# Optimization experiments

Measured on AMD Instinct MI355X. Metric: run time of the kernel, lower is better.

Reference implementation:

```python
import jax, jax.numpy as jnp
import numpy as np

H = 256; S = 64; AN = 16; D = 8; HH = 8; WW = 8; T = 32; N = 64; NV = 32
HG = 2 + 3 * H  # GRU hidden = sum(parser_sections) = 1 + 1 + 3*H


def _gru(x, w_ih, w_hh, b_ih, b_hh):
    """torch-style GRU over leading axis; x: [L, N, Hin] -> [L, N, HG]."""
    def step(h, xt):
        gi = xt @ w_ih.T + b_ih
        gh = h @ w_hh.T + b_hh
        ir, iz, inn = jnp.split(gi, 3, axis=-1)
        hr, hz, hn = jnp.split(gh, 3, axis=-1)
        r = jax.nn.sigmoid(ir + hr)
        z = jax.nn.sigmoid(iz + hz)
        n = jnp.tanh(inn + r * hn)
        h2 = (1 - z) * n + z * h
        return h2, h2
    h0 = jnp.zeros((x.shape[1], w_hh.shape[1]), x.dtype)
    _, ys = jax.lax.scan(step, h0, x)
    return ys


def _cos(e, m):  # e [N,H], m [N,S,H] -> [N,S]; matches F.cosine_similarity eps=1e-8
    num = jnp.einsum('nh,nsh->ns', e, m)
    den = jnp.linalg.norm(e, axis=-1)[:, None] * jnp.linalg.norm(m, axis=-1)
    return num / jnp.maximum(den, 1e-8)


def _l1norm(x):  # F.normalize(x, p=1, dim=-1)
    return x / jnp.maximum(jnp.abs(x).sum(-1, keepdims=True), 1e-12)


def setup_inputs():
    key = jax.random.key(0)
    ks = jax.random.split(key, 16)
    sc = lambda k, shape, fan: jax.random.normal(k, shape, jnp.float32) / np.float32(np.sqrt(fan))
    return dict(
        base=jax.random.normal(ks[0], (T, N, D, HH, WW), jnp.float32),
        interactable=(jax.random.uniform(ks[1], (T, N, AN - 5)) < 0.5).astype(jnp.float32),
        rnn_hxs=jnp.zeros((1, N, 1 + AN + 1 + H + S), jnp.float32),
        emb=sc(ks[2], (NV, H), 1.0),
        gru_w_ih=sc(ks[3], (3 * HG, H), H),
        gru_w_hh=sc(ks[4], (3 * HG, HG), HG),
        gru_b_ih=jnp.zeros((3 * HG,), jnp.float32),
        gru_b_hh=jnp.zeros((3 * HG,), jnp.float32),
        conv0_w=sc(ks[5], (H, D * H), D * H),
        conv0_b=jnp.zeros((H,), jnp.float32),
        convs_w=sc(ks[6], (2, H, H), H),
        convs_b=jnp.zeros((2, H), jnp.float32),
        lin_w=sc(ks[7], (H, H * HH * WW), H * HH * WW),
        lin_b=jnp.zeros((H,), jnp.float32),
        psi_w=sc(ks[8], (H, H * AN), H * AN),
        psi_b=jnp.zeros((H,), jnp.float32),
        actor_w=sc(ks[9], (AN, H), H),
        actor_b=jnp.zeros((AN,), jnp.float32),
        critic_w=sc(ks[10], (1, H), H),
        critic_b=jnp.zeros((1,), jnp.float32),
        subtasks=jax.random.randint(ks[11], (N, S), 0, NV),
        actions=jax.random.randint(ks[12], (T, N), 0, AN),
    )


def reference(base, interactable, rnn_hxs, emb, gru_w_ih, gru_w_hh, gru_b_ih, gru_b_hh,
              conv0_w, conv0_b, convs_w, convs_b, lin_w, lin_b, psi_w, psi_b,
              actor_w, actor_b, critic_w, critic_b, subtasks, actions):
    # --- parser: GRU over the subtask token sequence ---
    rnn_in = emb[subtasks].transpose(1, 0, 2)                                    # [S, N, H]
    X = _gru(rnn_in, gru_w_ih, gru_w_hh, gru_b_ih, gru_b_hh).transpose(1, 0, 2)  # [N, S, HG]
    c, p0 = X[..., 0], X[..., 1]                                                 # [N, S]
    M = X[..., 2:2 + H]
    Mm = X[..., 2 + H:2 + 2 * H]
    Mp = X[..., 2 + 2 * H:]
    hx = rnn_hxs[0]
    new_ep = jnp.all(rnn_hxs == 0, axis=-1)[0]                                   # [N]
    p_init = jnp.where(new_ep[:, None], p0, hx[:, 1 + AN + 1 + H:])

    def f_net(base_t, r):
        n = base_t.shape[0]
        # outer product [N,H,d,h,w] -> [N, H*d, h, w], then 1x1 convs
        x = (base_t[:, None] * r[:, :, None, None, None]).reshape(n, H * D, HH, WW)
        x = jax.nn.relu(jnp.einsum('nchw,oc->nohw', x, conv0_w) + conv0_b[None, :, None, None])
        for i in range(convs_w.shape[0]):
            x = jax.nn.relu(jnp.einsum('nchw,oc->nohw', x, convs_w[i]) + convs_b[i][None, :, None, None])
        return jax.nn.relu(x.reshape(n, -1) @ lin_w.T + lin_b)

    def step(p, xs):
        base_t, inter_t, a_t = xs
        ps = jax.nn.softmax(p, axis=-1)
        r = jnp.einsum('ns,nsh->nh', ps, M)                                      # memory read
        s = f_net(base_t, r)
        dprobs = jax.nn.softmax(s @ actor_w.T + actor_b, axis=-1)
        nonzero = jnp.pad(inter_t, ((0, 0), (5, 0)), constant_values=1.0)        # [N, AN]
        probs = dprobs * nonzero
        deficit = 1.0 - probs.sum(-1, keepdims=True)
        probs = probs + _l1norm(nonzero) * deficit
        probs = _l1norm(jnp.clip(probs, 0.0, 1.0))
        a_oh = jax.nn.one_hot(a_t, AN, dtype=s.dtype)
        e = (s[:, :, None] * a_oh[:, None, :]).reshape(s.shape[0], H * AN) @ psi_w.T + psi_b
        p_new = ps + c * _cos(e, Mp) - c * _cos(e, Mm)                           # memory write
        v = s @ critic_w.T + critic_b
        out = jnp.concatenate([a_t[:, None].astype(s.dtype), probs, v, s, p_new], axis=-1)
        return p_new, out

    _, hx_out = jax.lax.scan(step, p_init, (base, interactable, actions))        # [T, N, 338]
    return hx_out, hx_out[-1:]
```

## Files before the change

### kernel.cpp

```cpp
#include <hip/hip_runtime.h>
#include <math.h>

constexpr int cH  = 256;
constexpr int cS  = 64;
constexpr int cAN = 16;
constexpr int cD  = 8;
constexpr int cT  = 32;
constexpr int cN  = 64;
constexpr int cHG = 770;
constexpr int cG3 = 2310;
constexpr int cOW = 338;
constexpr int XLD = 800;
constexpr int GLD = 832;
constexpr int MLD = 2496;

__global__ __launch_bounds__(256) void k_gitab(const float* __restrict__ emb,
                                               const float* __restrict__ w_ih,
                                               const float* __restrict__ b_ih,
                                               float* __restrict__ gitp) {
  int v = blockIdx.y;
  int j = blockIdx.x * 256 + threadIdx.x;
  __shared__ float es[cH];
  es[threadIdx.x] = emb[v * cH + threadIdx.x];
  __syncthreads();
  if (j < cG3) {
    float acc = b_ih[j];
    const float* wr = w_ih + (size_t)j * cH;
    #pragma unroll 8
    for (int h = 0; h < cH; ++h) acc += wr[h] * es[h];
    int g = j / cHG, kk = j - g * cHG;
    gitp[(size_t)v * MLD + g * GLD + kk] = acc;
  }
}

__global__ __launch_bounds__(256) void k_wpad(const float* __restrict__ whh,
                                              float* __restrict__ wpadG) {
  int idx = blockIdx.x * 256 + threadIdx.x;
  if (idx < MLD * XLD) {
    int row = idx / XLD, col = idx - row * XLD;
    int g = row / GLD, k = row - g * GLD;
    wpadG[idx] = (k < cHG && col < cHG) ? whh[(size_t)(g * cHG + k) * cHG + col] : 0.f;
  }
}

__global__ __launch_bounds__(256) void k_psiperm(const float* __restrict__ psi_w,
                                                 float* __restrict__ psip) {
  int idx = blockIdx.x * 256 + threadIdx.x;
  int a = idx >> 16, h = (idx >> 8) & 255, o = idx & 255;
  psip[idx] = psi_w[((size_t)o * cH + h) * cAN + a];
}

__global__ __launch_bounds__(256) void k_gru_gemm(const float* __restrict__ wpadG,
                                                  const float* __restrict__ X,
                                                  float* __restrict__ part, int s) {
  int tid = threadIdx.x;
  int tile = blockIdx.x % 39;
  int ks   = blockIdx.x / 39;
  int g = tile / 13, kt = tile - g * 13;
  int cbase = (ks <= 2) ? ks * 13 : 38;
  int ccnt  = (ks < 2) ? 13 : 12;
  int kbase = cbase * 16;
  int csz = ccnt * 16;

  __shared__ float Bst[208][68];
  __shared__ float As[2][16][68];

  const float* bsrc = wpadG + ((size_t)(g * GLD + kt * 64)) * XLD + kbase;
  for (int i = tid; i < 64 * 208; i += 256) {
    int jl = i / 208, k2l = i - jl * 208;
    if (k2l < csz) Bst[k2l][jl] = bsrc[(size_t)jl * XLD + k2l];
  }

  int tm = tid & 15, tj = tid >> 4;
  int lrow = tid >> 2, lcol = (tid & 3) * 4;
  __syncthreads();

  float acc[4][4] = {};
  const float* Xp = X + ((size_t)lrow * cS + (s - 1)) * XLD + kbase;
  float4 av = *(const float4*)(Xp + lcol);
  for (int c = 0; c < ccnt; ++c) {
    int buf = c & 1;
    As[buf][lcol + 0][lrow] = av.x;
    As[buf][lcol + 1][lrow] = av.y;
    As[buf][lcol + 2][lrow] = av.z;
    As[buf][lcol + 3][lrow] = av.w;
    __syncthreads();
    if (c + 1 < ccnt) av = *(const float4*)(Xp + (c + 1) * 16 + lcol);
    #pragma unroll
    for (int kk = 0; kk < 16; ++kk) {
      float4 a4 = *(const float4*)&As[buf][kk][tm * 4];
      float4 b4 = *(const float4*)&Bst[c * 16 + kk][tj * 4];
      acc[0][0] += a4.x * b4.x; acc[0][1] += a4.x * b4.y; acc[0][2] += a4.x * b4.z; acc[0][3] += a4.x * b4.w;
      acc[1][0] += a4.y * b4.x; acc[1][1] += a4.y * b4.y; acc[1][2] += a4.y * b4.z; acc[1][3] += a4.y * b4.w;
      acc[2][0] += a4.z * b4.x; acc[2][1] += a4.z * b4.y; acc[2][2] += a4.z * b4.z; acc[2][3] += a4.z * b4.w;
      acc[3][0] += a4.w * b4.x; acc[3][1] += a4.w * b4.y; acc[3][2] += a4.w * b4.z; acc[3][3] += a4.w * b4.w;
    }
    __syncthreads();
  }
  float* pw = part + (size_t)ks * (64 * MLD) + (size_t)(g * GLD + kt * 64);
  #pragma unroll
  for (int i = 0; i < 4; ++i) {
    *(float4*)(pw + (size_t)(tm * 4 + i) * MLD + tj * 4) =
        make_float4(acc[i][0], acc[i][1], acc[i][2], acc[i][3]);
  }
}

__global__ __launch_bounds__(256) void k_gru_gate(const float* __restrict__ part,
                                                  const float* __restrict__ bhh,
                                                  const float* __restrict__ gitp,
                                                  const int* __restrict__ subtasks,
                                                  float* __restrict__ X, int s) {
  int kq = blockIdx.x, m = blockIdx.y, tid = threadIdx.x;
  if (tid >= 200) return;
  int k = kq * 200 + tid;
  float* xrow = X + ((size_t)m * cS + s) * XLD;
  if (k >= cHG) { xrow[k] = 0.f; return; }
  float accr = 0.f, accz = 0.f, accn = 0.f;
  if (s > 0) {
    const float* pm = part + (size_t)m * MLD;
    #pragma unroll
    for (int q = 0; q < 4; ++q) {
      const float* pq = pm + (size_t)q * (64 * MLD);
      accr += pq[k];
      accz += pq[GLD + k];
      accn += pq[2 * GLD + k];
    }
  }
  int v = subtasks[m * cS + s];
  const float* git = gitp + (size_t)v * MLD;
  float rg = 1.f / (1.f + expf(-(git[k]           + accr + bhh[k])));
  float zg = 1.f / (1.f + expf(-(git[GLD + k]     + accz + bhh[cHG + k])));
  float ng = tanhf(git[2 * GLD + k] + rg * (accn + bhh[2 * cHG + k]));
  float hp = (s > 0) ? X[((size_t)m * cS + (s - 1)) * XLD + k] : 0.f;
  xrow[k] = (1.f - zg) * ng + zg * hp;
}

__global__ __launch_bounds__(256) void k_pinit(const float* __restrict__ hxs,
                                               const float* __restrict__ X,
                                               float* __restrict__ psb,
                                               float* __restrict__ r,
                                               float* __restrict__ nMp,
                                               float* __restrict__ nMm) {
  int n = blockIdx.x, tid = threadIdx.x;
  __shared__ int anynz;
  __shared__ float pss[cS];
  __shared__ float mx, sm;
  if (tid == 0) anynz = 0;
  __syncthreads();
  int nz = (hxs[n * cOW + tid] != 0.f) ? 1 : 0;
  if (tid + 256 < cOW) nz |= (hxs[n * cOW + tid + 256] != 0.f) ? 1 : 0;
  if (nz) anynz = 1;
  __syncthreads();
  bool newep = (anynz == 0);
  if (tid < cS) {
    const float* xr = X + ((size_t)n * cS + tid) * XLD;
    float p0 = xr[1];
    float pv = newep ? p0 : hxs[n * cOW + 1 + cAN + 1 + cH + tid];
    pss[tid] = pv;
    float sp = 0.f, smn = 0.f;
    for (int h = 0; h < cH; ++h) {
      float vp = xr[2 + 2 * cH + h]; sp += vp * vp;
      float vm = xr[2 + cH + h];     smn += vm * vm;
    }
    nMp[n * cS + tid] = sqrtf(sp);
    nMm[n * cS + tid] = sqrtf(smn);
  }
  __syncthreads();
  if (tid == 0) { float m = pss[0]; for (int i = 1; i < cS; ++i) m = fmaxf(m, pss[i]); mx = m; }
  __syncthreads();
  if (tid < cS) pss[tid] = expf(pss[tid] - mx);
  __syncthreads();
  if (tid == 0) { float s = 0.f; for (int i = 0; i < cS; ++i) s += pss[i]; sm = s; }
  __syncthreads();
  if (tid < cS) { pss[tid] /= sm; psb[n * cS + tid] = pss[tid]; }
  __syncthreads();
  float acc = 0.f;
  for (int s2 = 0; s2 < cS; ++s2)
    acc += pss[s2] * X[((size_t)n * cS + s2) * XLD + 2 + tid];
  r[n * cH + tid] = acc;
}

__global__ __launch_bounds__(256) void k_front(const float* __restrict__ r,
                                               const float* __restrict__ base,
                                               const float* __restrict__ cw,
                                               const float* __restrict__ cb,
                                               float* __restrict__ x1T, int t) {
  int o = blockIdx.x, tid = threadIdx.x;
  __shared__ float rsQ[64][65][4];
  __shared__ float w0s[64][9];

  #pragma unroll
  for (int it = 0; it < 16; ++it) {
    int flat4 = it * 256 + tid;
    int n = flat4 >> 6, hq = flat4 & 63;
    float4 v = *(const float4*)(r + n * cH + hq * 4);
    *(float4*)&rsQ[hq][n][0] = v;
  }
  __syncthreads();

  {
    int dg = tid >> 6, n = tid & 63;
    int d0 = dg * 2;
    const float* cwo = cw + (size_t)o * (cD * cH);
    float acc0 = 0.f, acc1 = 0.f;
    #pragma unroll 4
    for (int hq = 0; hq < 64; ++hq) {
      float4 rv = *(const float4*)&rsQ[hq][n][0];
      #pragma unroll
      for (int j = 0; j < 4; ++j) {
        float2 w = *(const float2*)(cwo + (hq * 4 + j) * 8 + d0);
        float rvj = ((const float*)&rv)[j];
        acc0 += w.x * rvj;
        acc1 += w.y * rvj;
      }
    }
    w0s[n][d0]     = acc0;
    w0s[n][d0 + 1] = acc1;
  }
  __syncthreads();

  {
    int q = tid >> 6, n = tid & 63;
    float w0[8];
    #pragma unroll
    for (int d = 0; d < 8; ++d) w0[d] = w0s[n][d];
    float bias = cb[o];
    const float4* b4 = (const float4*)(base + ((size_t)(t * cN + n) * cD) * 64);
    float* dst = x1T + (size_t)o * 4096 + n * 64 + q * 16;
    #pragma unroll
    for (int k = 0; k < 4; ++k) {
      float4 acc = make_float4(bias, bias, bias, bias);
      #pragma unroll
      for (int d = 0; d < 8; ++d) {
        float4 bv = b4[d * 16 + q * 4 + k];
        acc.x += w0[d] * bv.x; acc.y += w0[d] * bv.y;
        acc.z += w0[d] * bv.z; acc.w += w0[d] * bv.w;
      }
      acc.x = fmaxf(acc.x, 0.f); acc.y = fmaxf(acc.y, 0.f);
      acc.z = fmaxf(acc.z, 0.f); acc.w = fmaxf(acc.w, 0.f);
      *(float4*)(dst + k * 4) = acc;
    }
  }
}

__global__ __launch_bounds__(256) void k_gemmT(const float* __restrict__ AT,
                                               const float* __restrict__ W,
                                               const float* __restrict__ bias,
                                               float* __restrict__ C, int mode) {
  int nb = blockIdx.x, mb = blockIdx.y, tid = threadIdx.x;
  int tm = tid & 15, tj = tid >> 4;
  __shared__ float As[16][68];
  __shared__ float Bs[16][68];
  float acc[4][4] = {{0.f}};
  int lrow = tid >> 2, lcol = (tid & 3) * 4;
  int kr = tid >> 4, mc4 = (tid & 15) * 4;
  for (int kc = 0; kc < cH; kc += 16) {
    float4 av = *(const float4*)(AT + (size_t)(kc + kr) * 4096 + mb * 64 + mc4);
    float4 wv = *(const float4*)(W + (size_t)(nb * 64 + lrow) * cH + kc + lcol);
    *(float4*)&As[kr][mc4] = av;
    Bs[lcol][lrow] = wv.x; Bs[lcol + 1][lrow] = wv.y; Bs[lcol + 2][lrow] = wv.z; Bs[lcol + 3][lrow] = wv.w;
    __syncthreads();
    #pragma unroll
    for (int kk = 0; kk < 16; ++kk) {
      float4 a4 = *(const float4*)&As[kk][tm * 4];
      float4 b4 = *(const float4*)&Bs[kk][tj * 4];
      acc[0][0] += a4.x * b4.x; acc[0][1] += a4.x * b4.y; acc[0][2] += a4.x * b4.z; acc[0][3] += a4.x * b4.w;
      acc[1][0] += a4.y * b4.x; acc[1][1] += a4.y * b4.y; acc[1][2] += a4.y * b4.z; acc[1][3] += a4.y * b4.w;
      acc[2][0] += a4.z * b4.x; acc[2][1] += a4.z * b4.y; acc[2][2] += a4.z * b4.z; acc[2][3] += a4.z * b4.w;
      acc[3][0] += a4.w * b4.x; acc[3][1] += a4.w * b4.y; acc[3][2] += a4.w * b4.z; acc[3][3] += a4.w * b4.w;
    }
    __syncthreads();
  }
  if (mode == 0) {
    #pragma unroll
    for (int j = 0; j < 4; ++j) {
      int o = nb * 64 + tj * 4 + j;
      float bv = bias[o];
      float4 o4;
      o4.x = fmaxf(acc[0][j] + bv, 0.f);
      o4.y = fmaxf(acc[1][j] + bv, 0.f);
      o4.z = fmaxf(acc[2][j] + bv, 0.f);
      o4.w = fmaxf(acc[3][j] + bv, 0.f);
      *(float4*)(C + (size_t)o * 4096 + mb * 64 + tm * 4) = o4;
    }
  } else {
    #pragma unroll
    for (int j = 0; j < 4; ++j) {
      int o = nb * 64 + tj * 4 + j;
      float bv = bias[o];
      float4 o4;
      o4.x = fmaxf(acc[0][j] + bv, 0.f);
      o4.y = fmaxf(acc[1][j] + bv, 0.f);
      o4.z = fmaxf(acc[2][j] + bv, 0.f);
      o4.w = fmaxf(acc[3][j] + bv, 0.f);
      *(float4*)(C + (size_t)mb * (64 * cH) + (size_t)o * 64 + tm * 4) = o4;
    }
  }
}

__global__ __launch_bounds__(256) void k_lin(const float* __restrict__ A,
                                             const float* __restrict__ W,
                                             float* __restrict__ part) {
  int nb = blockIdx.x, kcb = blockIdx.y, tid = threadIdx.x;
  int tm = tid & 15, tj = tid >> 4;
  __shared__ float As[16][68];
  __shared__ float Bs[16][68];
  float acc[4][4] = {{0.f}};
  int lrow = tid >> 2, lcol = (tid & 3) * 4;
  for (int kc = 0; kc < 256; kc += 16) {
    float4 av = *(const float4*)(A + (size_t)lrow * 16384 + kcb * 256 + kc + lcol);
    float4 wv = *(const float4*)(W + (size_t)(nb * 64 + lrow) * 16384 + kcb * 256 + kc + lcol);
    As[lcol][lrow] = av.x; As[lcol + 1][lrow] = av.y; As[lcol + 2][lrow] = av.z; As[lcol + 3][lrow] = av.w;
    Bs[lcol][lrow] = wv.x; Bs[lcol + 1][lrow] = wv.y; Bs[lcol + 2][lrow] = wv.z; Bs[lcol + 3][lrow] = wv.w;
    __syncthreads();
    #pragma unroll
    for (int kk = 0; kk < 16; ++kk) {
      float4 a4 = *(const float4*)&As[kk][tm * 4];
      float4 b4 = *(const float4*)&Bs[kk][tj * 4];
      acc[0][0] += a4.x * b4.x; acc[0][1] += a4.x * b4.y; acc[0][2] += a4.x * b4.z; acc[0][3] += a4.x * b4.w;
      acc[1][0] += a4.y * b4.x; acc[1][1] += a4.y * b4.y; acc[1][2] += a4.y * b4.z; acc[1][3] += a4.y * b4.w;
      acc[2][0] += a4.z * b4.x; acc[2][1] += a4.z * b4.y; acc[2][2] += a4.z * b4.z; acc[2][3] += a4.z * b4.w;
      acc[3][0] += a4.w * b4.x; acc[3][1] += a4.w * b4.y; acc[3][2] += a4.w * b4.z; acc[3][3] += a4.w * b4.w;
    }
    __syncthreads();
  }
  #pragma unroll
  for (int i = 0; i < 4; ++i) {
    int n = tm * 4 + i;
    float4 o4 = make_float4(acc[i][0], acc[i][1], acc[i][2], acc[i][3]);
    *(float4*)(part + ((size_t)kcb * cN + n) * cH + nb * 64 + tj * 4) = o4;
  }
}

__global__ __launch_bounds__(256) void k_tail(const float* __restrict__ part,
                                              const float* __restrict__ lin_b,
                                              const float* __restrict__ actor_w,
                                              const float* __restrict__ actor_b,
                                              const float* __restrict__ critic_w,
                                              const float* __restrict__ critic_b,
                                              const float* __restrict__ psip,
                                              const float* __restrict__ psi_b,
                                              const float* __restrict__ inter,
                                              const int* __restrict__ actions,
                                              const float* __restrict__ X,
                                              const float* __restrict__ nMp,
                                              const float* __restrict__ nMm,
                                              float* __restrict__ psb,
                                              float* __restrict__ r,
                                              float* __restrict__ out, int t) {
  int n = blockIdx.x, tid = threadIdx.x;
  __shared__ float ss[cH];
  __shared__ float es[cH];
  __shared__ float lg[cAN], dp[cAN], nzv[cAN], prb[cAN];
  __shared__ float red[256];
  __shared__ float ared[16][17];
  __shared__ float enorm_s;
  __shared__ float pns[cS];
  __shared__ float mx2, sm2;
  float* orow = out + ((size_t)t * cN + n) * cOW;
  float acc = lin_b[tid];
  for (int kc = 0; kc < 64; ++kc) acc += part[((size_t)kc * cN + n) * cH + tid];
  float sv = fmaxf(acc, 0.f);
  ss[tid] = sv;
  orow[1 + cAN + 1 + tid] = sv;
  __syncthreads();
  {
    int a = tid & 15, hg = tid >> 4;
    float pa = 0.f;
    const float* wr = actor_w + a * cH + hg * 16;
    const float* sh = &ss[hg * 16];
    #pragma unroll
    for (int hh2 = 0; hh2 < 16; ++hh2) pa += wr[hh2] * sh[hh2];
    ared[a][hg] = pa;
  }
  __syncthreads();
  if (tid < cAN) {
    float a = actor_b[tid];
    #pragma unroll
    for (int i = 0; i < 16; ++i) a += ared[tid][i];
    lg[tid] = a;
  }
  __syncthreads();
  if (tid < cAN) {
    float m = lg[0];
    for (int i = 1; i < cAN; ++i) m = fmaxf(m, lg[i]);
    dp[tid] = expf(lg[tid] - m);
  }
  __syncthreads();
  if (tid < cAN) {
    float s = 0.f;
    for (int i = 0; i < cAN; ++i) s += dp[i];
    float dprob = dp[tid] / s;
    float nv = (tid < 5) ? 1.f : inter[((size_t)t * cN + n) * (cAN - 5) + (tid - 5)];
    nzv[tid] = nv;
    prb[tid] = dprob * nv;
  }
  __syncthreads();
  if (tid < cAN) {
    float sp = 0.f, sn = 0.f;
    for (int i = 0; i < cAN; ++i) { sp += prb[i]; sn += nzv[i]; }
    float deficit = 1.f - sp;
    float v2 = prb[tid] + (nzv[tid] / fmaxf(sn, 1e-12f)) * deficit;
    prb[tid] = fminf(fmaxf(v2, 0.f), 1.f);
  }
  __syncthreads();
  if (tid < cAN) {
    float s = 0.f;
    for (int i = 0; i < cAN; ++i) s += prb[i];
    orow[1 + tid] = prb[tid] / fmaxf(s, 1e-12f);
  }
  int at = actions[t * cN + n];
  {
    float a = psi_b[tid];
    for (int h = 0; h < cH; ++h) a += psip[((size_t)at * cH + h) * cH + tid] * ss[h];
    es[tid] = a;
    red[tid] = a * a;
  }
  __syncthreads();
  for (int st = 128; st > 0; st >>= 1) {
    if (tid < st) red[tid] += red[tid + st];
    __syncthreads();
  }
  if (tid == 0) enorm_s = sqrtf(red[0]);
  __syncthreads();
  float enorm = enorm_s;
  red[tid] = critic_w[tid] * ss[tid];
  __syncthreads();
  for (int st = 128; st > 0; st >>= 1) {
    if (tid < st) red[tid] += red[tid + st];
    __syncthreads();
  }
  if (tid == 0) {
    orow[1 + cAN] = red[0] + critic_b[0];
    orow[0] = (float)at;
  }
  if (tid < cS) {
    const float* xr = X + ((size_t)n * cS + tid) * XLD;
    float dpp = 0.f, dmm = 0.f;
    for (int h = 0; h < cH; ++h) {
      float ev = es[h];
      dpp += ev * xr[2 + 2 * cH + h];
      dmm += ev * xr[2 + cH + h];
    }
    float cP = dpp / fmaxf(enorm * nMp[n * cS + tid], 1e-8f);
    float cM = dmm / fmaxf(enorm * nMm[n * cS + tid], 1e-8f);
    float cc = xr[0];
    float pn = psb[n * cS + tid] + cc * cP - cc * cM;
    pns[tid] = pn;
    orow[1 + cAN + 1 + cH + tid] = pn;
  }
  __threadfence_block();
  __syncthreads();
  if (t == cT - 1) {
    float* orow2 = out + (size_t)cT * cN * cOW + (size_t)n * cOW;
    orow2[tid] = orow[tid];
    if (tid + 256 < cOW) orow2[tid + 256] = orow[tid + 256];
  }
  if (tid == 0) { float m2 = pns[0]; for (int i = 1; i < cS; ++i) m2 = fmaxf(m2, pns[i]); mx2 = m2; }
  __syncthreads();
  if (tid < cS) pns[tid] = expf(pns[tid] - mx2);
  __syncthreads();
  if (tid == 0) { float s2 = 0.f; for (int i = 0; i < cS; ++i) s2 += pns[i]; sm2 = s2; }
  __syncthreads();
  if (tid < cS) { pns[tid] /= sm2; psb[n * cS + tid] = pns[tid]; }
  __syncthreads();
  float acc2 = 0.f;
  for (int s2 = 0; s2 < cS; ++s2)
    acc2 += pns[s2] * X[((size_t)n * cS + s2) * XLD + 2 + tid];
  r[n * cH + tid] = acc2;
}

extern "C" void kernel_launch(void* const* d_in, const int* in_sizes, int n_in,
                              void* d_out, int out_size, void* d_ws, size_t ws_size,
                              hipStream_t stream) {
  const float* base     = (const float*)d_in[0];
  const float* inter    = (const float*)d_in[1];
  const float* hxs      = (const float*)d_in[2];
  const float* emb      = (const float*)d_in[3];
  const float* w_ih     = (const float*)d_in[4];
  const float* w_hh     = (const float*)d_in[5];
  const float* b_ih     = (const float*)d_in[6];
  const float* b_hh     = (const float*)d_in[7];
  const float* conv0_w  = (const float*)d_in[8];
  const float* conv0_b  = (const float*)d_in[9];
  const float* convs_w  = (const float*)d_in[10];
  const float* convs_b  = (const float*)d_in[11];
  const float* lin_w    = (const float*)d_in[12];
  const float* lin_b    = (const float*)d_in[13];
  const float* psi_w    = (const float*)d_in[14];
  const float* psi_b    = (const float*)d_in[15];
  const float* actor_w  = (const float*)d_in[16];
  const float* actor_b  = (const float*)d_in[17];
  const float* critic_w = (const float*)d_in[18];
  const float* critic_b = (const float*)d_in[19];
  const int*   subtasks = (const int*)d_in[20];
  const int*   actions  = (const int*)d_in[21];
  float* out = (float*)d_out;
  float* ws  = (float*)d_ws;

  float* gitp  = ws + 0;
  float* psb   = ws + 0;
  float* r     = ws + 4096;
  float* nMp   = ws + 20480;
  float* nMm   = ws + 24576;
  float* X     = ws + 79872;
  float* wpadG = ws + 3356672;
  float* psip  = ws + 3356672;
  float* x1T   = ws + 4405248;
  float* part  = x1T;
  float* partG = ws + 5353472;
  float* x2T   = ws + 5453824;
  float* x3t   = ws + 6502400;

  k_gitab<<<dim3(10, 32), 256, 0, stream>>>(emb, w_ih, b_ih, gitp);
  k_wpad<<<7800, 256, 0, stream>>>(w_hh, wpadG);
  k_gru_gate<<<dim3(4, 64), 256, 0, stream>>>(partG, b_hh, gitp, subtasks, X, 0);
  for (int s = 1; s < cS; ++s) {
    k_gru_gemm<<<156, 256, 0, stream>>>(wpadG, X, partG, s);
    k_gru_gate<<<dim3(4, 64), 256, 0, stream>>>(partG, b_hh, gitp, subtasks, X, s);
  }
  k_psiperm<<<4096, 256, 0, stream>>>(psi_w, psip);
  k_pinit<<<64, 256, 0, stream>>>(hxs, X, psb, r, nMp, nMm);
  for (int t = 0; t < cT; ++t) {
    k_front<<<256, 256, 0, stream>>>(r, base, conv0_w, conv0_b, x1T, t);
    k_gemmT<<<dim3(4, 64), 256, 0, stream>>>(x1T, convs_w, convs_b, x2T, 0);
    k_gemmT<<<dim3(4, 64), 256, 0, stream>>>(x2T, convs_w + 65536, convs_b + 256, x3t, 1);
    k_lin<<<dim3(4, 64), 256, 0, stream>>>(x3t, lin_w, part);
    k_tail<<<64, 256, 0, stream>>>(part, lin_b, actor_w, actor_b, critic_w, critic_b,
                                   psip, psi_b, inter, actions, X, nMp, nMm,
                                   psb, r, out, t);
  }
}
```

Before: 4.732 ms.

## Fuse GRU recurrent GEMM and gate into one per-step kernel

Replaces the per-step split-K GEMM kernel plus separate gate kernel with a single kernel per timestep. Each block computes a 16-row by 64-column-per-gate tile with an in-block two-way K split, reduces it in shared memory and applies the GRU gates directly. This removes one launch per step and the global round trip of partial sums. The cost is far fewer blocks (52 instead of 156) and each block streaming a larger weight slice, so parallelism and latency hiding drop.

```diff
diff --git a/kernel.cpp b/kernel.cpp
--- a/kernel.cpp
+++ b/kernel.cpp
@@ -50,89 +50,127 @@
   psip[idx] = psi_w[((size_t)o * cH + h) * cAN + a];
 }
 
-__global__ __launch_bounds__(256) void k_gru_gemm(const float* __restrict__ wpadG,
-                                                  const float* __restrict__ X,
-                                                  float* __restrict__ part, int s) {
-  int tid = threadIdx.x;
-  int tile = blockIdx.x % 39;
-  int ks   = blockIdx.x / 39;
-  int g = tile / 13, kt = tile - g * 13;
-  int cbase = (ks <= 2) ? ks * 13 : 38;
-  int ccnt  = (ks < 2) ? 13 : 12;
-  int kbase = cbase * 16;
-  int csz = ccnt * 16;
-
-  __shared__ float Bst[208][68];
-  __shared__ float As[2][16][68];
-
-  const float* bsrc = wpadG + ((size_t)(g * GLD + kt * 64)) * XLD + kbase;
-  for (int i = tid; i < 64 * 208; i += 256) {
-    int jl = i / 208, k2l = i - jl * 208;
-    if (k2l < csz) Bst[k2l][jl] = bsrc[(size_t)jl * XLD + k2l];
-  }
-
-  int tm = tid & 15, tj = tid >> 4;
-  int lrow = tid >> 2, lcol = (tid & 3) * 4;
-  __syncthreads();
-
-  float acc[4][4] = {};
-  const float* Xp = X + ((size_t)lrow * cS + (s - 1)) * XLD + kbase;
-  float4 av = *(const float4*)(Xp + lcol);
-  for (int c = 0; c < ccnt; ++c) {
-    int buf = c & 1;
-    As[buf][lcol + 0][lrow] = av.x;
-    As[buf][lcol + 1][lrow] = av.y;
-    As[buf][lcol + 2][lrow] = av.z;
-    As[buf][lcol + 3][lrow] = av.w;
-    __syncthreads();
-    if (c + 1 < ccnt) av = *(const float4*)(Xp + (c + 1) * 16 + lcol);
-    #pragma unroll
-    for (int kk = 0; kk < 16; ++kk) {
-      float4 a4 = *(const float4*)&As[buf][kk][tm * 4];
-      float4 b4 = *(const float4*)&Bst[c * 16 + kk][tj * 4];
-      acc[0][0] += a4.x * b4.x; acc[0][1] += a4.x * b4.y; acc[0][2] += a4.x * b4.z; acc[0][3] += a4.x * b4.w;
-      acc[1][0] += a4.y * b4.x; acc[1][1] += a4.y * b4.y; acc[1][2] += a4.y * b4.z; acc[1][3] += a4.y * b4.w;
-      acc[2][0] += a4.z * b4.x; acc[2][1] += a4.z * b4.y; acc[2][2] += a4.z * b4.z; acc[2][3] += a4.z * b4.w;
-      acc[3][0] += a4.w * b4.x; acc[3][1] += a4.w * b4.y; acc[3][2] += a4.w * b4.z; acc[3][3] += a4.w * b4.w;
-    }
-    __syncthreads();
-  }
-  float* pw = part + (size_t)ks * (64 * MLD) + (size_t)(g * GLD + kt * 64);
-  #pragma unroll
-  for (int i = 0; i < 4; ++i) {
-    *(float4*)(pw + (size_t)(tm * 4 + i) * MLD + tj * 4) =
-        make_float4(acc[i][0], acc[i][1], acc[i][2], acc[i][3]);
-  }
-}
-
-__global__ __launch_bounds__(256) void k_gru_gate(const float* __restrict__ part,
+__global__ __launch_bounds__(256) void k_gru_step(const float* __restrict__ wpadG,
                                                   const float* __restrict__ bhh,
                                                   const float* __restrict__ gitp,
                                                   const int* __restrict__ subtasks,
                                                   float* __restrict__ X, int s) {
-  int kq = blockIdx.x, m = blockIdx.y, tid = threadIdx.x;
-  if (tid >= 200) return;
-  int k = kq * 200 + tid;
-  float* xrow = X + ((size_t)m * cS + s) * XLD;
-  if (k >= cHG) { xrow[k] = 0.f; return; }
-  float accr = 0.f, accz = 0.f, accn = 0.f;
+  int tid = threadIdx.x;
+  int kt = blockIdx.x % 13, mq = blockIdx.x / 13;
+  int ksub = tid >> 7, t = tid & 127;
+
+  __shared__ float As[2][2][16][20];
+  __shared__ float Bs[2][2][16][200];
+  __shared__ float gh[16][200];
+
+  float acc[4][6] = {};
+  int tm = t >> 5, tj = t & 31;
+
   if (s > 0) {
-    const float* pm = part + (size_t)m * MLD;
-    #pragma unroll
-    for (int q = 0; q < 4; ++q) {
-      const float* pq = pm + (size_t)q * (64 * MLD);
-      accr += pq[k];
-      accz += pq[GLD + k];
-      accn += pq[2 * GLD + k];
-    }
-  }
-  int v = subtasks[m * cS + s];
-  const float* git = gitp + (size_t)v * MLD;
-  float rg = 1.f / (1.f + expf(-(git[k]           + accr + bhh[k])));
-  float zg = 1.f / (1.f + expf(-(git[GLD + k]     + accz + bhh[cHG + k])));
-  float ng = tanhf(git[2 * GLD + k] + rg * (accn + bhh[2 * cHG + k]));
-  float hp = (s > 0) ? X[((size_t)m * cS + (s - 1)) * XLD + k] : 0.f;
-  xrow[k] = (1.f - zg) * ng + zg * hp;
+    int kbase = ksub * 400;
+    int lm = t >> 2, lq = t & 3;
+    int bjl[6], bq[6];
+    const float* brow[6];
+    #pragma unroll
+    for (int i = 0; i < 6; ++i) {
+      int idx = i * 128 + t;
+      int jl = idx % 192, q = idx / 192;
+      bjl[i] = jl; bq[i] = q;
+      int g = jl >> 6, jj = jl & 63;
+      brow[i] = wpadG + (size_t)(g * GLD + kt * 64 + jj) * XLD + kbase + q * 4;
+    }
+    const float* arow = (t < 64)
+        ? X + ((size_t)(mq * 16 + lm) * cS + (s - 1)) * XLD + kbase + lq * 4
+        : nullptr;
+
+    float4 pa = make_float4(0.f, 0.f, 0.f, 0.f);
+    float4 pb[6];
+    if (t < 64) pa = *(const float4*)(arow);
+    #pragma unroll
+    for (int i = 0; i < 6; ++i) pb[i] = *(const float4*)(brow[i]);
+
+    for (int c = 0; c < 25; ++c) {
+      int buf = c & 1;
+      if (t < 64) {
+        As[buf][ksub][lq * 4 + 0][lm] = pa.x;
+        As[buf][ksub][lq * 4 + 1][lm] = pa.y;
+        As[buf][ksub][lq * 4 + 2][lm] = pa.z;
+        As[buf][ksub][lq * 4 + 3][lm] = pa.w;
+      }
+      #pragma unroll
+      for (int i = 0; i < 6; ++i) {
+        int r0 = bq[i] * 4, jl = bjl[i];
+        Bs[buf][ksub][r0 + 0][jl] = pb[i].x;
+        Bs[buf][ksub][r0 + 1][jl] = pb[i].y;
+        Bs[buf][ksub][r0 + 2][jl] = pb[i].z;
+        Bs[buf][ksub][r0 + 3][jl] = pb[i].w;
+      }
+      __syncthreads();
+      if (c + 1 < 25) {
+        if (t < 64) pa = *(const float4*)(arow + (c + 1) * 16);
+        #pragma unroll
+        for (int i = 0; i < 6; ++i) pb[i] = *(const float4*)(brow[i] + (c + 1) * 16);
+      }
+      #pragma unroll
+      for (int k2 = 0; k2 < 16; ++k2) {
+        float4 a4 = *(const float4*)&As[buf][ksub][k2][tm * 4];
+        const float* br = &Bs[buf][ksub][k2][tj * 6];
+        float2 b01 = *(const float2*)(br);
+        float2 b23 = *(const float2*)(br + 2);
+        float2 b45 = *(const float2*)(br + 4);
+        acc[0][0] += a4.x * b01.x; acc[0][1] += a4.x * b01.y; acc[0][2] += a4.x * b23.x;
+        acc[0][3] += a4.x * b23.y; acc[0][4] += a4.x * b45.x; acc[0][5] += a4.x * b45.y;
+        acc[1][0] += a4.y * b01.x; acc[1][1] += a4.y * b01.y; acc[1][2] += a4.y * b23.x;
+        acc[1][3] += a4.y * b23.y; acc[1][4] += a4.y * b45.x; acc[1][5] += a4.y * b45.y;
+        acc[2][0] += a4.z * b01.x; acc[2][1] += a4.z * b01.y; acc[2][2] += a4.z * b23.x;
+        acc[2][3] += a4.z * b23.y; acc[2][4] += a4.z * b45.x; acc[2][5] += a4.z * b45.y;
+        acc[3][0] += a4.w * b01.x; acc[3][1] += a4.w * b01.y; acc[3][2] += a4.w * b23.x;
+        acc[3][3] += a4.w * b23.y; acc[3][4] += a4.w * b45.x; acc[3][5] += a4.w * b45.y;
+      }
+      __syncthreads();
+    }
+    if (ksub == 1) {
+      #pragma unroll
+      for (int i = 0; i < 4; ++i)
+        #pragma unroll
+        for (int j = 0; j < 6; ++j) gh[tm * 4 + i][tj * 6 + j] = acc[i][j];
+    }
+    __syncthreads();
+    if (ksub == 0) {
+      #pragma unroll
+      for (int i = 0; i < 4; ++i)
+        #pragma unroll
+        for (int j = 0; j < 6; ++j) gh[tm * 4 + i][tj * 6 + j] += acc[i][j];
+    }
+    __syncthreads();
+  }
+
+  {
+    int m = tid >> 4, jq = (tid & 15) * 4;
+    int mg = mq * 16 + m;
+    float* xrow = X + ((size_t)mg * cS + s) * XLD;
+    const float* xprev = X + ((size_t)mg * cS + (s > 0 ? s - 1 : 0)) * XLD;
+    int v = subtasks[mg * cS + s];
+    const float* git = gitp + (size_t)v * MLD;
+    #pragma unroll
+    for (int i = 0; i < 4; ++i) {
+      int jj = jq + i;
+      int kglob = kt * 64 + jj;
+      if (kglob >= XLD) continue;
+      if (kglob >= cHG) { xrow[kglob] = 0.f; continue; }
+      float accr = 0.f, accz = 0.f, accn = 0.f;
+      if (s > 0) {
+        accr = gh[m][jj];
+        accz = gh[m][64 + jj];
+        accn = gh[m][128 + jj];
+      }
+      float rg = 1.f / (1.f + expf(-(git[kglob]           + accr + bhh[kglob])));
+      float zg = 1.f / (1.f + expf(-(git[GLD + kglob]     + accz + bhh[cHG + kglob])));
+      float ng = tanhf(git[2 * GLD + kglob] + rg * (accn + bhh[2 * cHG + kglob]));
+      float hp = (s > 0) ? xprev[kglob] : 0.f;
+      xrow[kglob] = (1.f - zg) * ng + zg * hp;
+    }
+  }
 }
 
 __global__ __launch_bounds__(256) void k_pinit(const float* __restrict__ hxs,
@@ -508,17 +546,13 @@
   float* psip  = ws + 3356672;
   float* x1T   = ws + 4405248;
   float* part  = x1T;
-  float* partG = ws + 5353472;
   float* x2T   = ws + 5453824;
   float* x3t   = ws + 6502400;
 
   k_gitab<<<dim3(10, 32), 256, 0, stream>>>(emb, w_ih, b_ih, gitp);
   k_wpad<<<7800, 256, 0, stream>>>(w_hh, wpadG);
-  k_gru_gate<<<dim3(4, 64), 256, 0, stream>>>(partG, b_hh, gitp, subtasks, X, 0);
-  for (int s = 1; s < cS; ++s) {
-    k_gru_gemm<<<156, 256, 0, stream>>>(wpadG, X, partG, s);
-    k_gru_gate<<<dim3(4, 64), 256, 0, stream>>>(partG, b_hh, gitp, subtasks, X, s);
-  }
+  for (int s = 0; s < cS; ++s)
+    k_gru_step<<<52, 256, 0, stream>>>(wpadG, b_hh, gitp, subtasks, X, s);
   k_psiperm<<<4096, 256, 0, stream>>>(psi_w, psip);
   k_pinit<<<64, 256, 0, stream>>>(hxs, X, psb, r, nMp, nMm);
   for (int t = 0; t < cT; ++t) {
```

Result: slower. 6.118 ms (+29.3%).
